# Kernel tuning notes

Measured on AMD Instinct MI355X. Metric: run time of the kernel, lower is better.

The kernel has to match this reference:

```python
import jax, jax.numpy as jnp
import numpy as np

N = 500000      # data points
D = 64          # n_in
NS = 128        # N_samples


def setup_inputs() -> dict:
    key = jax.random.key(0)
    k1, k2, k3, k4 = jax.random.split(key, 4)
    X = jax.random.normal(k1, (N, D), dtype=jnp.float32)
    w_mu = jax.random.normal(k2, (D,), dtype=jnp.float32)
    w_log_var = jax.random.normal(k3, (D,), dtype=jnp.float32)
    z = jax.random.normal(k4, (NS,), dtype=jnp.float32)  # z_i samples
    return {"X": X, "w_mu": w_mu, "w_log_var": w_log_var, "z": z}


def reference(X, w_mu, w_log_var, z):
    # mean_i = X @ w_mu                       [N]
    mean_i = X @ w_mu
    # std_i = sqrt(diag(X diag(exp(lv)) X^T)) == sqrt(sum_j X_ij^2 * exp(lv_j))
    var_i = jnp.einsum('nd,d->n', X * X, jnp.exp(w_log_var))  # [N]
    std_i = jnp.sqrt(var_i)
    # activation_mat[i, s] = std_i * z_s + mean_i          [N, NS]
    activation_mat = std_i[:, None] * z[None, :] + mean_i[:, None]
    return jax.nn.sigmoid(activation_mat)
```

## Files before the change

### kernel.cpp

```cpp
#include <hip/hip_runtime.h>
#include <math.h>


__global__ __launch_bounds__(256) void logreg_sample_kernel(
    const float* __restrict__ X,
    const float* __restrict__ w_mu,
    const float* __restrict__ w_lv,
    const float* __restrict__ z,
    float* __restrict__ out,
    int n_rows)
{
    const int tid   = blockIdx.x * blockDim.x + threadIdx.x;
    const int row   = tid >> 4;
    const int l     = tid & 15;
    if (row >= n_rows) return;

    const float4 mu4 = ((const float4*)w_mu)[l];
    const float4 lv4 = ((const float4*)w_lv)[l];
    const float4 ev4 = make_float4(__expf(lv4.x), __expf(lv4.y),
                                   __expf(lv4.z), __expf(lv4.w));
    const float4 z0 = ((const float4*)z)[l];
    const float4 z1 = ((const float4*)z)[16 + l];

    const float4 x4 = ((const float4*)X)[row * 16 + l];

    float a = x4.x * mu4.x + x4.y * mu4.y + x4.z * mu4.z + x4.w * mu4.w;
    float b = x4.x * x4.x * ev4.x + x4.y * x4.y * ev4.y
            + x4.z * x4.z * ev4.z + x4.w * x4.w * ev4.w;

    #pragma unroll
    for (int m = 1; m < 16; m <<= 1) {
        a += __shfl_xor(a, m, 64);
        b += __shfl_xor(b, m, 64);
    }
    const float mean = a;
    const float stdv = sqrtf(b);

    float4 o0, o1;
    o0.x = 1.0f / (1.0f + __expf(-(stdv * z0.x + mean)));
    o0.y = 1.0f / (1.0f + __expf(-(stdv * z0.y + mean)));
    o0.z = 1.0f / (1.0f + __expf(-(stdv * z0.z + mean)));
    o0.w = 1.0f / (1.0f + __expf(-(stdv * z0.w + mean)));
    o1.x = 1.0f / (1.0f + __expf(-(stdv * z1.x + mean)));
    o1.y = 1.0f / (1.0f + __expf(-(stdv * z1.y + mean)));
    o1.z = 1.0f / (1.0f + __expf(-(stdv * z1.z + mean)));
    o1.w = 1.0f / (1.0f + __expf(-(stdv * z1.w + mean)));

    float4* orow = (float4*)(out + (size_t)row * 128);
    orow[l]      = o0;
    orow[16 + l] = o1;
}

extern "C" void kernel_launch(void* const* d_in, const int* in_sizes, int n_in,
                              void* d_out, int out_size, void* d_ws, size_t ws_size,
                              hipStream_t stream) {
    const float* X    = (const float*)d_in[0];
    const float* w_mu = (const float*)d_in[1];
    const float* w_lv = (const float*)d_in[2];
    const float* z    = (const float*)d_in[3];
    float* out = (float*)d_out;

    const int n_rows = in_sizes[0] / 64;
    const int total_threads = n_rows * 16;
    const int blocks = (total_threads + 255) / 256;

    logreg_sample_kernel<<<blocks, 256, 0, stream>>>(X, w_mu, w_lv, z, out, n_rows);
}
```

Before: 334.6 us.

## Use grid-stride loop with prefetch, nontemporal loads/stores, and fast reciprocal sigmoid

Replaces the one-row-per-16-thread-group launch with a persistent grid-stride loop over 2048 blocks. Each group prefetches the next row of X while it computes the current one. X loads and output stores become nontemporal to avoid polluting the cache with streamed data. The sigmoid division is replaced by a hardware reciprocal approximation. Fewer blocks may reduce latency hiding, and the nontemporal hints could change write-combining behaviour on this bandwidth-bound kernel.

```diff
diff --git a/kernel.cpp b/kernel.cpp
--- a/kernel.cpp
+++ b/kernel.cpp
@@ -1,6 +1,12 @@
 #include <hip/hip_runtime.h>
 #include <math.h>
 
+
+typedef float f4 __attribute__((ext_vector_type(4)));
+
+__device__ __forceinline__ float sigmoid_fast(float t) {
+    return __builtin_amdgcn_rcpf(1.0f + __expf(-t));
+}
 
 __global__ __launch_bounds__(256) void logreg_sample_kernel(
     const float* __restrict__ X,
@@ -10,45 +16,62 @@
     float* __restrict__ out,
     int n_rows)
 {
-    const int tid   = blockIdx.x * blockDim.x + threadIdx.x;
-    const int row   = tid >> 4;
-    const int l     = tid & 15;
+    const int tid  = blockIdx.x * blockDim.x + threadIdx.x;
+    const int grp  = tid >> 4;
+    const int l    = tid & 15;
+    const int ngrp = (gridDim.x * blockDim.x) >> 4;
+
+    const f4 mu4 = ((const f4*)w_mu)[l];
+    const f4 lv4 = ((const f4*)w_lv)[l];
+    f4 ev4;
+    ev4[0] = __expf(lv4[0]); ev4[1] = __expf(lv4[1]);
+    ev4[2] = __expf(lv4[2]); ev4[3] = __expf(lv4[3]);
+    const f4 z0 = ((const f4*)z)[l];
+    const f4 z1 = ((const f4*)z)[16 + l];
+
+    int row = grp;
     if (row >= n_rows) return;
 
-    const float4 mu4 = ((const float4*)w_mu)[l];
-    const float4 lv4 = ((const float4*)w_lv)[l];
-    const float4 ev4 = make_float4(__expf(lv4.x), __expf(lv4.y),
-                                   __expf(lv4.z), __expf(lv4.w));
-    const float4 z0 = ((const float4*)z)[l];
-    const float4 z1 = ((const float4*)z)[16 + l];
+    const f4* Xv = (const f4*)X;
 
-    const float4 x4 = ((const float4*)X)[row * 16 + l];
+    f4 xc = __builtin_nontemporal_load(&Xv[(size_t)row * 16 + l]);
 
-    float a = x4.x * mu4.x + x4.y * mu4.y + x4.z * mu4.z + x4.w * mu4.w;
-    float b = x4.x * x4.x * ev4.x + x4.y * x4.y * ev4.y
-            + x4.z * x4.z * ev4.z + x4.w * x4.w * ev4.w;
+    while (row < n_rows) {
+        const int nrow = row + ngrp;
+        f4 xn = {0.0f, 0.0f, 0.0f, 0.0f};
+        if (nrow < n_rows)
+            xn = __builtin_nontemporal_load(&Xv[(size_t)nrow * 16 + l]);
 
-    #pragma unroll
-    for (int m = 1; m < 16; m <<= 1) {
-        a += __shfl_xor(a, m, 64);
-        b += __shfl_xor(b, m, 64);
+        float a = xc[0] * mu4[0] + xc[1] * mu4[1]
+                + xc[2] * mu4[2] + xc[3] * mu4[3];
+        float b = xc[0] * xc[0] * ev4[0] + xc[1] * xc[1] * ev4[1]
+                + xc[2] * xc[2] * ev4[2] + xc[3] * xc[3] * ev4[3];
+
+        #pragma unroll
+        for (int m = 1; m < 16; m <<= 1) {
+            a += __shfl_xor(a, m, 64);
+            b += __shfl_xor(b, m, 64);
+        }
+        const float mean = a;
+        const float stdv = sqrtf(b);
+
+        f4 o0, o1;
+        o0[0] = sigmoid_fast(stdv * z0[0] + mean);
+        o0[1] = sigmoid_fast(stdv * z0[1] + mean);
+        o0[2] = sigmoid_fast(stdv * z0[2] + mean);
+        o0[3] = sigmoid_fast(stdv * z0[3] + mean);
+        o1[0] = sigmoid_fast(stdv * z1[0] + mean);
+        o1[1] = sigmoid_fast(stdv * z1[1] + mean);
+        o1[2] = sigmoid_fast(stdv * z1[2] + mean);
+        o1[3] = sigmoid_fast(stdv * z1[3] + mean);
+
+        f4* orow = (f4*)(out + (size_t)row * 128);
+        __builtin_nontemporal_store(o0, orow + l);
+        __builtin_nontemporal_store(o1, orow + 16 + l);
+
+        xc  = xn;
+        row = nrow;
     }
-    const float mean = a;
-    const float stdv = sqrtf(b);
-
-    float4 o0, o1;
-    o0.x = 1.0f / (1.0f + __expf(-(stdv * z0.x + mean)));
-    o0.y = 1.0f / (1.0f + __expf(-(stdv * z0.y + mean)));
-    o0.z = 1.0f / (1.0f + __expf(-(stdv * z0.z + mean)));
-    o0.w = 1.0f / (1.0f + __expf(-(stdv * z0.w + mean)));
-    o1.x = 1.0f / (1.0f + __expf(-(stdv * z1.x + mean)));
-    o1.y = 1.0f / (1.0f + __expf(-(stdv * z1.y + mean)));
-    o1.z = 1.0f / (1.0f + __expf(-(stdv * z1.z + mean)));
-    o1.w = 1.0f / (1.0f + __expf(-(stdv * z1.w + mean)));
-
-    float4* orow = (float4*)(out + (size_t)row * 128);
-    orow[l]      = o0;
-    orow[16 + l] = o1;
 }
 
 extern "C" void kernel_launch(void* const* d_in, const int* in_sizes, int n_in,
@@ -61,8 +84,10 @@
     float* out = (float*)d_out;
 
     const int n_rows = in_sizes[0] / 64;
-    const int total_threads = n_rows * 16;
-    const int blocks = (total_threads + 255) / 256;
+    const int threads = 256;
+    int blocks = 2048;
+    long long need = ((long long)n_rows * 16 + threads - 1) / threads;
+    if (need < blocks) blocks = (int)need;
 
-    logreg_sample_kernel<<<blocks, 256, 0, stream>>>(X, w_mu, w_lv, z, out, n_rows);
+    logreg_sample_kernel<<<blocks, threads, 0, stream>>>(X, w_mu, w_lv, z, out, n_rows);
 }
```

Measured after the change: 339.0 us, median of 2. About the same (+1.3%).
